# Kernel tuning notes

Measured on AMD Instinct MI355X. Metric: run time of the kernel, lower is better.

The kernel has to match this reference:

```python
import jax, jax.numpy as jnp
import numpy as np

NEG_SLOPE = 0.01  # torch F.leaky_relu default


def _gat_stack(x, W, a1w, a1b, a2w, a2b):
    """One GAT stack over all heads.
    x: (B, N, F_in); W: (H, F_in, d); a1w/a2w: (H, d); a1b/a2b: (H,)
    returns (B, N, H*d) -- heads concatenated in order along last dim.
    """
    # 1x1 conv1d (no bias) == per-node linear projection
    fts = jnp.einsum('bnf,hfd->hbnd', x, W)                      # (H,B,N,d)
    f1 = jnp.einsum('hbnd,hd->hbn', fts, a1w) + a1b[:, None, None]
    f2 = jnp.einsum('hbnd,hd->hbn', fts, a2w) + a2b[:, None, None]
    # logits[h,b,i,j] = f1[h,b,i] + f2[h,b,j]  (f_1.permute + f_2 broadcast)
    logits = f1[:, :, :, None] + f2[:, :, None, :]               # (H,B,N,N)
    coefs = jax.nn.softmax(jax.nn.leaky_relu(logits, NEG_SLOPE), axis=-1)
    vals = jnp.einsum('hbnm,hbmd->hbnd', coefs, fts)             # bmm aggregation
    ret = jax.nn.elu(vals + fts)                                 # residual-within-head + ELU activation
    B, N = x.shape[0], x.shape[1]
    return jnp.transpose(ret, (1, 2, 0, 3)).reshape(B, N, -1)    # cat(heads, dim=-1)


def setup_inputs() -> dict:
    key = jax.random.key(0)
    ks = jax.random.split(key, 7)
    B, N, F_in, H, d = 32, 512, 128, 8, 64
    hidden = H * d  # 512
    s = 0.05
    return {
        'x':   jax.random.normal(ks[0], (B, N, F_in), jnp.float32),
        'W0':  jax.random.normal(ks[1], (H, F_in, d), jnp.float32) * s,
        'W1':  jax.random.normal(ks[2], (H, hidden, d), jnp.float32) * s,
        'a1w': jax.random.normal(ks[3], (2, H, d), jnp.float32) * s,
        'a1b': jax.random.normal(ks[4], (2, H), jnp.float32) * s,
        'a2w': jax.random.normal(ks[5], (2, H, d), jnp.float32) * s,
        'a2b': jax.random.normal(ks[6], (2, H), jnp.float32) * s,
    }


def reference(x, W0, W1, a1w, a1b, a2w, a2b):
    # stack 0: input dim = num_random_sample
    h = _gat_stack(x, W0, a1w[0], a1b[0], a2w[0], a2b[0])
    # stack 1: input dim = hidden_dim
    out = _gat_stack(h, W1, a1w[1], a1b[1], a2w[1], a2b[1])
    return out
```

## Files before the change

### kernel.cpp

```cpp
#include <hip/hip_runtime.h>
#include <hip/hip_bf16.h>
#include <stdint.h>

typedef __attribute__((ext_vector_type(8))) short short8;
typedef __attribute__((ext_vector_type(4))) float f32x4;

#define L2E 1.44269504f
#define FN  131072

__device__ __forceinline__ short f2bf(float f) {
    unsigned u = __builtin_bit_cast(unsigned, f);
    return (short)((u + 0x8000u) >> 16);
}
__device__ __forceinline__ float bf2f(short s) {
    unsigned u = ((unsigned)(unsigned short)s) << 16;
    return __builtin_bit_cast(float, u);
}

__device__ __forceinline__ void gld16(void* l, const void* g) {
    __builtin_amdgcn_global_load_lds(
        (const __attribute__((address_space(1))) unsigned*)g,
        (__attribute__((address_space(3))) unsigned*)l, 16, 0, 0);
}

#define PIPE_OPEN()  do { __builtin_amdgcn_s_barrier();                        \
                          __builtin_amdgcn_sched_barrier(0);                   \
                          asm volatile("" ::: "memory"); } while (0)
#define PIPE_CLOSE() do { asm volatile("s_waitcnt lgkmcnt(0)" ::: "memory");   \
                          __builtin_amdgcn_sched_barrier(0);                   \
                          __builtin_amdgcn_s_barrier(); } while (0)

__global__ void wtrans_kernel(const float* __restrict__ W0, const float* __restrict__ W1,
                              short* __restrict__ BT0, short* __restrict__ BT1) {
    int idx = blockIdx.x * 256 + threadIdx.x;
    if (idx < 8 * 128 * 64) {
        int h = idx >> 13;
        int k = (idx >> 6) & 127;
        int dd = idx & 63;
        BT0[(h * 64 + dd) * 128 + k] = f2bf(W0[idx]);
    } else {
        int j = idx - 8 * 128 * 64;
        int h = j >> 15;
        int k = (j >> 6) & 511;
        int dd = j & 63;
        BT1[(h * 64 + dd) * 512 + k] = f2bf(W1[j]);
    }
}

template <typename AT>
__global__ __launch_bounds__(256, 2)
void gemm_kernel(const AT* __restrict__ A, const short* __restrict__ BT,
                 short* __restrict__ fts, int K,
                 const float* __restrict__ a1w, const float* __restrict__ a1b,
                 const float* __restrict__ a2w, const float* __restrict__ a2b,
                 float* __restrict__ fbuf) {
    __shared__ __align__(16) short As[2][128 * 64];
    __shared__ __align__(16) short Bs[2][128 * 64];

    const int tid  = threadIdx.x;
    const int lane = tid & 63;
    const int w    = tid >> 6;
    const int wr   = w >> 1, wc = w & 1;
    const int quad = lane >> 4, l15 = lane & 15;

    const int id = blockIdx.x;
    const int bx = (id >> 3) & 3;
    const int by = ((id >> 5) << 3) + (id & 7);
    const int m0 = by * 128;
    const int n0 = bx * 128;

    const int rl   = lane >> 3;
    const int cpos = lane & 7;
    const int kcl  = cpos ^ rl;

    f32x4 acc[4][4];
    for (int i = 0; i < 4; ++i)
        for (int j = 0; j < 4; ++j) { f32x4 z = {0.f, 0.f, 0.f, 0.f}; acc[i][j] = z; }

    const int nkb = K >> 6;

    if constexpr (sizeof(AT) == 4) {
        for (int kb = 0; kb < nkb; ++kb) {
            __syncthreads();
            for (int i = 0; i < 8; ++i) {
                int id2 = tid + i * 256;
                int row = id2 >> 4, q = id2 & 15;
                int c = q >> 1, half = q & 1;
                float4 v = *(const float4*)((const float*)A + (size_t)(m0 + row) * K + kb * 64 + q * 4);
                ushort4 p;
                p.x = (unsigned short)f2bf(v.x);
                p.y = (unsigned short)f2bf(v.y);
                p.z = (unsigned short)f2bf(v.z);
                p.w = (unsigned short)f2bf(v.w);
                int swz = c ^ (row & 7);
                *(ushort4*)(As[0] + row * 64 + swz * 8 + half * 4) = p;
            }
            for (int i = 0; i < 4; ++i) {
                int rowb = w * 32 + i * 8;
                gld16(Bs[0] + rowb * 64,
                      BT + (size_t)(n0 + rowb + rl) * K + kb * 64 + kcl * 8);
            }
            __syncthreads();
            short8 af[2][4], bf[2][4];
            for (int ks = 0; ks < 2; ++ks) {
                for (int mf = 0; mf < 4; ++mf) {
                    int row = wr * 64 + mf * 16 + l15;
                    af[ks][mf] = *(const short8*)(As[0] + row * 64 + (((ks * 4 + quad) ^ (row & 7)) << 3));
                }
                for (int nf = 0; nf < 4; ++nf) {
                    int row = wc * 64 + nf * 16 + l15;
                    bf[ks][nf] = *(const short8*)(Bs[0] + row * 64 + (((ks * 4 + quad) ^ (row & 7)) << 3));
                }
            }
            for (int ks = 0; ks < 2; ++ks)
                for (int mf = 0; mf < 4; ++mf)
                    for (int nf = 0; nf < 4; ++nf)
                        acc[mf][nf] = __builtin_amdgcn_mfma_f32_16x16x32_bf16(af[ks][mf], bf[ks][nf], acc[mf][nf], 0, 0, 0);
        }
    } else {
        auto stageAB = [&](int kb, int bufi) {
#pragma unroll
            for (int i = 0; i < 4; ++i) {
                int rowb = w * 32 + i * 8;
                gld16(As[bufi] + rowb * 64,
                      (const short*)A + (size_t)(m0 + rowb + rl) * K + kb * 64 + kcl * 8);
            }
#pragma unroll
            for (int i = 0; i < 4; ++i) {
                int rowb = w * 32 + i * 8;
                gld16(Bs[bufi] + rowb * 64,
                      BT + (size_t)(n0 + rowb + rl) * K + kb * 64 + kcl * 8);
            }
        };
        stageAB(0, 0);
        if (nkb > 1) stageAB(1, 1);
        for (int kb = 0; kb < nkb; ++kb) {
            if (kb + 1 < nkb) asm volatile("s_waitcnt vmcnt(8)" ::: "memory");
            else              asm volatile("s_waitcnt vmcnt(0)" ::: "memory");
            PIPE_OPEN();
            const short* as = As[kb & 1];
            const short* bs = Bs[kb & 1];
            short8 af[2][4], bf[2][4];
            for (int ks = 0; ks < 2; ++ks) {
                for (int mf = 0; mf < 4; ++mf) {
                    int row = wr * 64 + mf * 16 + l15;
                    af[ks][mf] = *(const short8*)(as + row * 64 + (((ks * 4 + quad) ^ (row & 7)) << 3));
                }
                for (int nf = 0; nf < 4; ++nf) {
                    int row = wc * 64 + nf * 16 + l15;
                    bf[ks][nf] = *(const short8*)(bs + row * 64 + (((ks * 4 + quad) ^ (row & 7)) << 3));
                }
            }
            for (int ks = 0; ks < 2; ++ks)
                for (int mf = 0; mf < 4; ++mf)
                    for (int nf = 0; nf < 4; ++nf)
                        acc[mf][nf] = __builtin_amdgcn_mfma_f32_16x16x32_bf16(af[ks][mf], bf[ks][nf], acc[mf][nf], 0, 0, 0);
            PIPE_CLOSE();
            if (kb + 2 < nkb) stageAB(kb + 2, kb & 1);
        }
    }

    for (int nf = 0; nf < 4; ++nf) {
        int col = n0 + wc * 64 + nf * 16 + l15;
        int h = col >> 6, dd = col & 63;
        for (int mf = 0; mf < 4; ++mf) {
            int m = m0 + wr * 64 + mf * 16 + quad * 4;
            int b = m >> 9, n = m & 511;
            ushort4 pk;
            pk.x = (unsigned short)f2bf(acc[mf][nf][0]);
            pk.y = (unsigned short)f2bf(acc[mf][nf][1]);
            pk.z = (unsigned short)f2bf(acc[mf][nf][2]);
            pk.w = (unsigned short)f2bf(acc[mf][nf][3]);
            *(ushort4*)(fts + (size_t)((h * 32 + b) * 64 + dd) * 512 + n) = pk;
        }
    }

    {
        const int head = (n0 >> 6) + wc;
        float w1[4], w2[4];
        for (int nf = 0; nf < 4; ++nf) {
            w1[nf] = a1w[head * 64 + nf * 16 + l15];
            w2[nf] = a2w[head * 64 + nf * 16 + l15];
        }
        const float b1 = a1b[head], b2 = a2b[head];
        const int rsel = l15 & 3;
        for (int mf = 0; mf < 4; ++mf) {
            float g1[4], g2[4];
            for (int r = 0; r < 4; ++r) {
                float s1 = 0.f, s2 = 0.f;
                for (int nf = 0; nf < 4; ++nf) {
                    s1 += acc[mf][nf][r] * w1[nf];
                    s2 += acc[mf][nf][r] * w2[nf];
                }
                for (int m = 1; m < 16; m <<= 1) {
                    s1 += __shfl_xor(s1, m, 64);
                    s2 += __shfl_xor(s2, m, 64);
                }
                g1[r] = s1; g2[r] = s2;
            }
            float v1 = rsel == 0 ? g1[0] : rsel == 1 ? g1[1] : rsel == 2 ? g1[2] : g1[3];
            float v2 = rsel == 0 ? g2[0] : rsel == 1 ? g2[1] : rsel == 2 ? g2[2] : g2[3];
            if (l15 < 4) {
                int m = m0 + wr * 64 + mf * 16 + quad * 4 + rsel;
                int b = m >> 9, i = m & 511;
                int fi = (head * 32 + b) * 512 + i;
                float f1 = v1 + b1, f2 = v2 + b2;
                fbuf[0 * FN + fi] = __builtin_amdgcn_exp2f(f1 * L2E);
                fbuf[1 * FN + fi] = __builtin_amdgcn_exp2f(f1 * (0.01f * L2E));
                fbuf[2 * FN + fi] = __builtin_amdgcn_exp2f(f2 * L2E);
                fbuf[3 * FN + fi] = __builtin_amdgcn_exp2f(f2 * (0.01f * L2E));
            }
        }
    }
}

template <typename OutT>
__global__ __launch_bounds__(256, 4)
void attn_kernel(const short* __restrict__ fts, const float* __restrict__ fbuf,
                 OutT* __restrict__ out) {
    __shared__ __align__(16) short fb0[64 * 128];
    __shared__ __align__(16) short fb1[64 * 128];
    __shared__ __align__(16) float p2_s[512];
    __shared__ __align__(16) float q2_s[512];

    const int tid  = threadIdx.x;
    const int lane = tid & 63, w = tid >> 6;
    const int quad = lane >> 4, l15 = lane & 15;
    const int bx   = blockIdx.x;
    const int quarter = bx >> 8;
    const int slab = bx & 255;
    const int h    = slab >> 5;
    const int b    = slab & 31;
    const int r0   = quarter * 128;
    const size_t fbase = (size_t)(slab * 64) * 512;
    const int fidx = slab * 512;

    const int srow = lane >> 4;
    const int spc  = lane & 15;

    f32x4 acc[2][4], accL[2];
    for (int i = 0; i < 2; ++i) {
        f32x4 z = {0.f, 0.f, 0.f, 0.f};
        accL[i] = z;
        for (int j = 0; j < 4; ++j) acc[i][j] = z;
    }
    short8 onesv;
    for (int t = 0; t < 8; ++t) onesv[t] = (short)0x3F80;

    float P1r[2], Q1r[2];
    for (int rt = 0; rt < 2; ++rt) {
        int i = fidx + r0 + w * 32 + rt * 16 + l15;
        P1r[rt] = fbuf[i];
        Q1r[rt] = fbuf[1 * FN + i];
    }

    const float* p2g = fbuf + 2 * FN + fidx;
    const float* q2g = fbuf + 3 * FN + fidx;

    if (w < 2) gld16(p2_s + w * 256, p2g + w * 256 + lane * 4);
    else       gld16(q2_s + (w - 2) * 256, q2g + (w - 2) * 256 + lane * 4);

    auto stage = [&](int tc, short* buf) {
#pragma unroll
        for (int i = 0; i < 4; ++i) {
            int d0 = w * 16 + i * 4;
            int d  = d0 + srow;
            gld16(buf + d0 * 128,
                  fts + fbase + (size_t)d * 512 + tc * 128 + ((spc ^ (d & 7)) << 3));
        }
    };
    stage(0, fb0);
    stage(1, fb1);

#pragma unroll
    for (int tc = 0; tc < 4; ++tc) {
        if (tc < 3) asm volatile("s_waitcnt vmcnt(4)" ::: "memory");
        else        asm volatile("s_waitcnt vmcnt(0)" ::: "memory");
        PIPE_OPEN();

        const short* buf = (tc & 1) ? fb1 : fb0;
#pragma unroll
        for (int jb = 0; jb < 4; ++jb) {
            short8 bfr[4];
#pragma unroll
            for (int nf = 0; nf < 4; ++nf) {
                int col = nf * 16 + l15;
                bfr[nf] = *(const short8*)(buf + col * 128 + (((jb * 4 + quad) ^ (col & 7)) << 3));
            }
            int o = tc * 128 + jb * 32 + quad * 8;
            f32x4 pa = *(const f32x4*)(p2_s + o), pb = *(const f32x4*)(p2_s + o + 4);
            f32x4 qa = *(const f32x4*)(q2_s + o), qb = *(const f32x4*)(q2_s + o + 4);
            float p2v[8] = {pa[0], pa[1], pa[2], pa[3], pb[0], pb[1], pb[2], pb[3]};
            float q2v[8] = {qa[0], qa[1], qa[2], qa[3], qb[0], qb[1], qb[2], qb[3]};

#pragma unroll
            for (int rt = 0; rt < 2; ++rt) {
                short8 ef;
#pragma unroll
                for (int t = 0; t < 8; ++t)
                    ef[t] = f2bf(fmaxf(P1r[rt] * p2v[t], Q1r[rt] * q2v[t]));
                for (int nf = 0; nf < 4; ++nf)
                    acc[rt][nf] = __builtin_amdgcn_mfma_f32_16x16x32_bf16(ef, bfr[nf], acc[rt][nf], 0, 0, 0);
                accL[rt] = __builtin_amdgcn_mfma_f32_16x16x32_bf16(ef, onesv, accL[rt], 0, 0, 0);
            }
        }

        PIPE_CLOSE();
        if (tc == 0) stage(2, fb0);
        if (tc == 1) stage(3, fb1);
    }

    for (int rt = 0; rt < 2; ++rt) {
        float rinv[4];
        for (int r = 0; r < 4; ++r) rinv[r] = __builtin_amdgcn_rcpf(accL[rt][r]);
        int i0 = r0 + w * 32 + rt * 16 + quad * 4;
        for (int nf = 0; nf < 4; ++nf) {
            int col = nf * 16 + l15;
            ushort4 res = *(const ushort4*)(fts + fbase + col * 512 + i0);
            unsigned short rr[4] = {res.x, res.y, res.z, res.w};
            for (int r = 0; r < 4; ++r) {
                float val = acc[rt][nf][r] * rinv[r] + bf2f((short)rr[r]);
                if (val < 0.f) val = __builtin_amdgcn_exp2f(val * L2E) - 1.f;
                size_t oidx = (size_t)(b * 512 + i0 + r) * 512 + h * 64 + col;
                if constexpr (sizeof(OutT) == 4) out[oidx] = val;
                else                             out[oidx] = f2bf(val);
            }
        }
    }
}

extern "C" void kernel_launch(void* const* d_in, const int* in_sizes, int n_in,
                              void* d_out, int out_size, void* d_ws, size_t ws_size,
                              hipStream_t stream) {
    const float* x   = (const float*)d_in[0];
    const float* W0  = (const float*)d_in[1];
    const float* W1  = (const float*)d_in[2];
    const float* a1w = (const float*)d_in[3];
    const float* a1b = (const float*)d_in[4];
    const float* a2w = (const float*)d_in[5];
    const float* a2b = (const float*)d_in[6];
    float* out = (float*)d_out;

    char* ws = (char*)d_ws;
    short* BT0  = (short*)(ws);
    short* BT1  = (short*)(ws + 131072);
    float* fbuf = (float*)(ws + 655360);
    short* fts  = (short*)(ws + 2752512);
    short* hbuf = (short*)d_out;

    wtrans_kernel<<<1280, 256, 0, stream>>>(W0, W1, BT0, BT1);

    gemm_kernel<float><<<512, 256, 0, stream>>>(x, BT0, fts, 128,
                                                a1w, a1b, a2w, a2b, fbuf);
    attn_kernel<short><<<1024, 256, 0, stream>>>(fts, fbuf, hbuf);

    gemm_kernel<short><<<512, 256, 0, stream>>>(hbuf, BT1, fts, 512,
                                                a1w + 512, a1b + 8, a2w + 512, a2b + 8, fbuf);
    attn_kernel<float><<<1024, 256, 0, stream>>>(fts, fbuf, out);
}
```

Baseline: 145.4 us.

## Split attention blocks into 64-row eighths with 64-column staging chunks

Each attention block now covers 64 query rows (one 16-row tile per wave) instead of 128, doubling the grid to 2048 blocks. The V staging chunks shrink to 64 columns, which halves LDS per block, and launch bounds rise to allow 6 blocks per CU. The goal is higher occupancy and better latency hiding. In exchange, every block re-reads the full fts slab for half as many rows, doubling global/L2 traffic per output row, and each wave issues fewer MFMAs per load.

Result: slower. 164.5 us (+13.2%).

```diff
diff --git a/kernel.cpp b/kernel.cpp
--- a/kernel.cpp
+++ b/kernel.cpp
@@ -215,11 +215,11 @@
 }
 
 template <typename OutT>
-__global__ __launch_bounds__(256, 4)
+__global__ __launch_bounds__(256, 6)
 void attn_kernel(const short* __restrict__ fts, const float* __restrict__ fbuf,
                  OutT* __restrict__ out) {
-    __shared__ __align__(16) short fb0[64 * 128];
-    __shared__ __align__(16) short fb1[64 * 128];
+    __shared__ __align__(16) short fb0[64 * 64];
+    __shared__ __align__(16) short fb1[64 * 64];
     __shared__ __align__(16) float p2_s[512];
     __shared__ __align__(16) float q2_s[512];
 
@@ -227,31 +227,31 @@
     const int lane = tid & 63, w = tid >> 6;
     const int quad = lane >> 4, l15 = lane & 15;
     const int bx   = blockIdx.x;
-    const int quarter = bx >> 8;
-    const int slab = bx & 255;
+    const int slab   = bx >> 3;
+    const int eighth = bx & 7;
     const int h    = slab >> 5;
     const int b    = slab & 31;
-    const int r0   = quarter * 128;
+    const int r0   = eighth * 64;
     const size_t fbase = (size_t)(slab * 64) * 512;
     const int fidx = slab * 512;
 
-    const int srow = lane >> 4;
-    const int spc  = lane & 15;
-
-    f32x4 acc[2][4], accL[2];
-    for (int i = 0; i < 2; ++i) {
+    const int rl  = lane >> 3;
+    const int spc = lane & 7;
+
+    f32x4 acc[4], accL;
+    {
         f32x4 z = {0.f, 0.f, 0.f, 0.f};
-        accL[i] = z;
-        for (int j = 0; j < 4; ++j) acc[i][j] = z;
+        accL = z;
+        for (int j = 0; j < 4; ++j) acc[j] = z;
     }
     short8 onesv;
     for (int t = 0; t < 8; ++t) onesv[t] = (short)0x3F80;
 
-    float P1r[2], Q1r[2];
-    for (int rt = 0; rt < 2; ++rt) {
-        int i = fidx + r0 + w * 32 + rt * 16 + l15;
-        P1r[rt] = fbuf[i];
-        Q1r[rt] = fbuf[1 * FN + i];
+    float P1, Q1;
+    {
+        int i = fidx + r0 + w * 16 + l15;
+        P1 = fbuf[i];
+        Q1 = fbuf[1 * FN + i];
     }
 
     const float* p2g = fbuf + 2 * FN + fidx;
@@ -262,64 +262,60 @@
 
     auto stage = [&](int tc, short* buf) {
 #pragma unroll
-        for (int i = 0; i < 4; ++i) {
-            int d0 = w * 16 + i * 4;
-            int d  = d0 + srow;
-            gld16(buf + d0 * 128,
-                  fts + fbase + (size_t)d * 512 + tc * 128 + ((spc ^ (d & 7)) << 3));
+        for (int i = 0; i < 2; ++i) {
+            int d0 = (w * 2 + i) * 8;
+            int d  = d0 + rl;
+            gld16(buf + d0 * 64,
+                  fts + fbase + (size_t)d * 512 + tc * 64 + ((spc ^ rl) << 3));
         }
     };
     stage(0, fb0);
     stage(1, fb1);
 
 #pragma unroll
-    for (int tc = 0; tc < 4; ++tc) {
-        if (tc < 3) asm volatile("s_waitcnt vmcnt(4)" ::: "memory");
+    for (int tc = 0; tc < 8; ++tc) {
+        if (tc < 7) asm volatile("s_waitcnt vmcnt(2)" ::: "memory");
         else        asm volatile("s_waitcnt vmcnt(0)" ::: "memory");
         PIPE_OPEN();
 
-        const short* buf = (tc & 1) ? fb1 : fb0;
-#pragma unroll
-        for (int jb = 0; jb < 4; ++jb) {
+        short* buf = (tc & 1) ? fb1 : fb0;
+#pragma unroll
+        for (int jb = 0; jb < 2; ++jb) {
             short8 bfr[4];
 #pragma unroll
             for (int nf = 0; nf < 4; ++nf) {
                 int col = nf * 16 + l15;
-                bfr[nf] = *(const short8*)(buf + col * 128 + (((jb * 4 + quad) ^ (col & 7)) << 3));
-            }
-            int o = tc * 128 + jb * 32 + quad * 8;
+                bfr[nf] = *(const short8*)(buf + col * 64 + (((jb * 4 + quad) ^ (col & 7)) << 3));
+            }
+            int o = tc * 64 + jb * 32 + quad * 8;
             f32x4 pa = *(const f32x4*)(p2_s + o), pb = *(const f32x4*)(p2_s + o + 4);
             f32x4 qa = *(const f32x4*)(q2_s + o), qb = *(const f32x4*)(q2_s + o + 4);
             float p2v[8] = {pa[0], pa[1], pa[2], pa[3], pb[0], pb[1], pb[2], pb[3]};
             float q2v[8] = {qa[0], qa[1], qa[2], qa[3], qb[0], qb[1], qb[2], qb[3]};
 
-#pragma unroll
-            for (int rt = 0; rt < 2; ++rt) {
-                short8 ef;
-#pragma unroll
-                for (int t = 0; t < 8; ++t)
-                    ef[t] = f2bf(fmaxf(P1r[rt] * p2v[t], Q1r[rt] * q2v[t]));
-                for (int nf = 0; nf < 4; ++nf)
-                    acc[rt][nf] = __builtin_amdgcn_mfma_f32_16x16x32_bf16(ef, bfr[nf], acc[rt][nf], 0, 0, 0);
-                accL[rt] = __builtin_amdgcn_mfma_f32_16x16x32_bf16(ef, onesv, accL[rt], 0, 0, 0);
-            }
+            short8 ef;
+#pragma unroll
+            for (int t = 0; t < 8; ++t)
+                ef[t] = f2bf(fmaxf(P1 * p2v[t], Q1 * q2v[t]));
+            for (int nf = 0; nf < 4; ++nf)
+                acc[nf] = __builtin_amdgcn_mfma_f32_16x16x32_bf16(ef, bfr[nf], acc[nf], 0, 0, 0);
+            accL = __builtin_amdgcn_mfma_f32_16x16x32_bf16(ef, onesv, accL, 0, 0, 0);
         }
 
         PIPE_CLOSE();
-        if (tc == 0) stage(2, fb0);
-        if (tc == 1) stage(3, fb1);
-    }
-
-    for (int rt = 0; rt < 2; ++rt) {
+        if (tc + 2 < 8) stage(tc + 2, buf);
+    }
+
+    {
         float rinv[4];
-        for (int r = 0; r < 4; ++r) rinv[r] = __builtin_amdgcn_rcpf(accL[rt][r]);
-        int i0 = r0 + w * 32 + rt * 16 + quad * 4;
+        for (int r = 0; r < 4; ++r) rinv[r] = __builtin_amdgcn_rcpf(accL[r]);
+        int i0 = r0 + w * 16 + quad * 4;
         for (int nf = 0; nf < 4; ++nf) {
             int col = nf * 16 + l15;
             ushort4 res = *(const ushort4*)(fts + fbase + col * 512 + i0);
             unsigned short rr[4] = {res.x, res.y, res.z, res.w};
             for (int r = 0; r < 4; ++r) {
-                float val = acc[rt][nf][r] * rinv[r] + bf2f((short)rr[r]);
+                float val = acc[nf][r] * rinv[r] + bf2f((short)rr[r]);
                 if (val < 0.f) val = __builtin_amdgcn_exp2f(val * L2E) - 1.f;
                 size_t oidx = (size_t)(b * 512 + i0 + r) * 512 + h * 64 + col;
                 if constexpr (sizeof(OutT) == 4) out[oidx] = val;
@@ -352,9 +348,9 @@
 
     gemm_kernel<float><<<512, 256, 0, stream>>>(x, BT0, fts, 128,
                                                 a1w, a1b, a2w, a2b, fbuf);
-    attn_kernel<short><<<1024, 256, 0, stream>>>(fts, fbuf, hbuf);
+    attn_kernel<short><<<2048, 256, 0, stream>>>(fts, fbuf, hbuf);
 
     gemm_kernel<short><<<512, 256, 0, stream>>>(hbuf, BT1, fts, 512,
                                                 a1w + 512, a1b + 8, a2w + 512, a2b + 8, fbuf);
-    attn_kernel<float><<<1024, 256, 0, stream>>>(fts, fbuf, out);
-}
+    attn_kernel<float><<<2048, 256, 0, stream>>>(fts, fbuf, out);
+}
```
